# Performance work log

Hardware: AMD Instinct MI355X
Metric: run time of the kernel (lower is better)

The kernel has to match this reference:

```python
import jax, jax.numpy as jnp
import numpy as np

N_RADIAL = 8
N_ATOMS = 250000
# tril_2d_indices(n_radial): all (i, j) pairs with i >= j (includes diagonal)
TRIL_I, TRIL_J = np.tril_indices(N_RADIAL)
N_TRIL = TRIL_I.shape[0]  # 36
N_SYMM01_FEATURES = N_TRIL * N_RADIAL  # 288


def setup_inputs() -> dict:
    key = jax.random.key(0)
    k1, k2 = jax.random.split(key)
    # moments[1]: first-order moment [n_atoms, n_radial, 3]
    m1 = jax.random.normal(k1, (N_ATOMS, N_RADIAL, 3), dtype=jnp.float32)
    # moments[2]: second-order moment [n_atoms, n_radial, 3, 3]
    m2 = jax.random.normal(k2, (N_ATOMS, N_RADIAL, 3, 3), dtype=jnp.float32)
    return {"m1": m1, "m2": m2}


def reference(m1, m2):
    # contr_num = 5: contr[r, s, t, a] = sum_{i,j} m1[a,r,i] * m1[a,s,j] * m2[a,t,i,j]
    contr = jnp.einsum("ari,asj,atij->rsta", m1, m1, m2)  # [R, R, R, A]
    # use_full_contrs_5_6 branch: gather lower-triangular (r, s) pairs, then
    # flatten to [-1, n_tril * n_radial] exactly as the original module does.
    gm = contr[TRIL_I, TRIL_J]                       # [N_TRIL, R, A]
    gm = jnp.reshape(gm, (-1, N_SYMM01_FEATURES))    # [A, 288]
    return gm
```

## Files before the change

kernel.cpp:

```cpp
#include <hip/hip_runtime.h>

#define N_ATOMS 250000
#define NR 8
#define BLK 512
#define NP 36
#define NBLK ((N_ATOMS + BLK - 1) / BLK)

typedef float f4 __attribute__((ext_vector_type(4)));

__global__ __launch_bounds__(BLK, 4) void moment_contr_kernel(
    const float* __restrict__ m1,
    const float* __restrict__ m2,
    float* __restrict__ out)
{
    __shared__ float sbuf[BLK / 64][NP][64];

    const int orig = blockIdx.x;
    const int q = NBLK / 8, r = NBLK % 8;
    const int xcd = orig & 7;
    const int wgid = (xcd < r ? xcd * (q + 1)
                              : r * (q + 1) + (xcd - r) * q) + (orig >> 3);

    const int tid  = threadIdx.x;
    const int wid  = tid >> 6;
    const int lane = tid & 63;
    const long long wbase = (long long)wgid * BLK + (long long)wid * 64;
    const long long a = wbase + lane;
    const bool live = (a < N_ATOMS);

    float (*swave)[64] = sbuf[wid];

    float m1v[24];
    if (live) {
        const f4* p = reinterpret_cast<const f4*>(m1 + (size_t)a * 24);
        #pragma unroll
        for (int k = 0; k < 6; ++k) {
            f4 v = p[k];
            m1v[4*k+0] = v.x; m1v[4*k+1] = v.y;
            m1v[4*k+2] = v.z; m1v[4*k+3] = v.w;
        }
    } else {
        #pragma unroll
        for (int k = 0; k < 24; ++k) m1v[k] = 0.f;
    }

    const float* m2a = m2 + (size_t)a * 72;

    #pragma unroll
    for (int th = 0; th < 2; ++th) {
        float m2h[36];
        if (live) {
            const f4* ph = reinterpret_cast<const f4*>(m2a + th * 36);
            #pragma unroll
            for (int k = 0; k < 9; ++k) {
                f4 v = ph[k];
                m2h[4*k+0] = v.x; m2h[4*k+1] = v.y;
                m2h[4*k+2] = v.z; m2h[4*k+3] = v.w;
            }
        } else {
            #pragma unroll
            for (int k = 0; k < 36; ++k) m2h[k] = 0.f;
        }

        #pragma unroll
        for (int t4 = 0; t4 < 4; ++t4) {
            const int t = th * 4 + t4;

            float B[24];
            #pragma unroll
            for (int s = 0; s < NR; ++s) {
                #pragma unroll
                for (int i = 0; i < 3; ++i) {
                    B[s*3+i] = m1v[s*3+0] * m2h[t4*9 + i*3 + 0]
                             + m1v[s*3+1] * m2h[t4*9 + i*3 + 1]
                             + m1v[s*3+2] * m2h[t4*9 + i*3 + 2];
                }
            }

            #pragma unroll
            for (int rr = 0; rr < NR; ++rr) {
                #pragma unroll
                for (int s = 0; s <= rr; ++s) {
                    const int p = rr*(rr+1)/2 + s;
                    swave[p][lane] = m1v[rr*3+0] * B[s*3+0]
                                   + m1v[rr*3+1] * B[s*3+1]
                                   + m1v[rr*3+2] * B[s*3+2];
                }
            }

            asm volatile("s_waitcnt lgkmcnt(0)" ::: "memory");

            #pragma unroll
            for (int it = 0; it < 9; ++it) {
                const int p   = it * 4 + (lane >> 4);
                const int sub = (4 * lane) & 63;
                if (wbase + sub + 4 <= N_ATOMS) {
                    f4 v = *reinterpret_cast<const f4*>(&swave[p][sub]);
                    __builtin_nontemporal_store(
                        v, reinterpret_cast<f4*>(
                            out + (size_t)p * (NR * N_ATOMS)
                                + (size_t)t * N_ATOMS + wbase + sub));
                }
            }
        }
    }
}

extern "C" void kernel_launch(void* const* d_in, const int* in_sizes, int n_in,
                              void* d_out, int out_size, void* d_ws, size_t ws_size,
                              hipStream_t stream) {
    const float* m1 = (const float*)d_in[0];
    const float* m2 = (const float*)d_in[1];
    float* out = (float*)d_out;

    hipLaunchKernelGGL(moment_contr_kernel, dim3(NBLK), dim3(BLK), 0, stream,
                       m1, m2, out);
}
```

Baseline: 75.14 us.

## Share staging buffer across block so each wave stores whole 2KB output rows

Replaces the per-wave shared staging buffer with one block-wide buffer indexed by thread id. After a block barrier, each wave writes a subset of the 36 pair rows across all 512 atoms, so every global store run covers 2KB contiguous instead of 256B. This costs two block-wide barriers per t iteration and lowers the launch-bounds occupancy hint from 4 to 2, so there is less overlap between waves.

After: 73.71 us. About the same (-1.9%).

```diff
diff --git a/kernel.cpp b/kernel.cpp
--- a/kernel.cpp
+++ b/kernel.cpp
@@ -8,12 +8,12 @@
 
 typedef float f4 __attribute__((ext_vector_type(4)));
 
-__global__ __launch_bounds__(BLK, 4) void moment_contr_kernel(
+__global__ __launch_bounds__(BLK, 2) void moment_contr_kernel(
     const float* __restrict__ m1,
     const float* __restrict__ m2,
     float* __restrict__ out)
 {
-    __shared__ float sbuf[BLK / 64][NP][64];
+    __shared__ float sbuf[NP][BLK];
 
     const int orig = blockIdx.x;
     const int q = NBLK / 8, r = NBLK % 8;
@@ -24,18 +24,19 @@
     const int tid  = threadIdx.x;
     const int wid  = tid >> 6;
     const int lane = tid & 63;
-    const long long wbase = (long long)wgid * BLK + (long long)wid * 64;
-    const long long a = wbase + lane;
+    const long long block_base = (long long)wgid * BLK;
+    const long long a = block_base + tid;
     const bool live = (a < N_ATOMS);
 
-    float (*swave)[64] = sbuf[wid];
+    const int pstart = (wid < 4) ? 5 * wid : 20 + 4 * (wid - 4);
+    const int pcnt   = (wid < 4) ? 5 : 4;
 
     float m1v[24];
     if (live) {
-        const f4* p = reinterpret_cast<const f4*>(m1 + (size_t)a * 24);
+        const f4* p1 = reinterpret_cast<const f4*>(m1 + (size_t)a * 24);
         #pragma unroll
         for (int k = 0; k < 6; ++k) {
-            f4 v = p[k];
+            f4 v = p1[k];
             m1v[4*k+0] = v.x; m1v[4*k+1] = v.y;
             m1v[4*k+2] = v.z; m1v[4*k+3] = v.w;
         }
@@ -82,26 +83,33 @@
                 #pragma unroll
                 for (int s = 0; s <= rr; ++s) {
                     const int p = rr*(rr+1)/2 + s;
-                    swave[p][lane] = m1v[rr*3+0] * B[s*3+0]
-                                   + m1v[rr*3+1] * B[s*3+1]
-                                   + m1v[rr*3+2] * B[s*3+2];
+                    sbuf[p][tid] = m1v[rr*3+0] * B[s*3+0]
+                                 + m1v[rr*3+1] * B[s*3+1]
+                                 + m1v[rr*3+2] * B[s*3+2];
                 }
             }
 
-            asm volatile("s_waitcnt lgkmcnt(0)" ::: "memory");
+            asm volatile("s_waitcnt lgkmcnt(0)\n\ts_barrier" ::: "memory");
 
-            #pragma unroll
-            for (int it = 0; it < 9; ++it) {
-                const int p   = it * 4 + (lane >> 4);
-                const int sub = (4 * lane) & 63;
-                if (wbase + sub + 4 <= N_ATOMS) {
-                    f4 v = *reinterpret_cast<const f4*>(&swave[p][sub]);
-                    __builtin_nontemporal_store(
-                        v, reinterpret_cast<f4*>(
-                            out + (size_t)p * (NR * N_ATOMS)
-                                + (size_t)t * N_ATOMS + wbase + sub));
+            for (int k = 0; k < 5; ++k) {
+                if (k < pcnt) {
+                    const int p = pstart + k;
+                    #pragma unroll
+                    for (int half = 0; half < 2; ++half) {
+                        const int sub = half * 256 + 4 * lane;
+                        const long long g = block_base + sub;
+                        if (g + 4 <= N_ATOMS) {
+                            f4 v = *reinterpret_cast<const f4*>(&sbuf[p][sub]);
+                            __builtin_nontemporal_store(
+                                v, reinterpret_cast<f4*>(
+                                    out + (size_t)p * (NR * N_ATOMS)
+                                        + (size_t)t * N_ATOMS + g));
+                        }
+                    }
                 }
             }
+
+            asm volatile("s_barrier" ::: "memory");
         }
     }
 }
```
